# Kernel optimization log

Measured on AMD Instinct MI355X. Metric: run time of the kernel, lower is better.

The kernel has to match this reference:

```python
import jax, jax.numpy as jnp
import numpy as np

NEG_SLOPE_GAT = 0.2   # PyG GATConv default negative_slope
NEG_SLOPE_ACT = 0.01  # torch F.leaky_relu default


def gat_conv(x, src, dst, W, att_src, att_dst, b, N):
    # Single-head PyG GATConv with self-loops already appended in (src, dst).
    xl = x @ W                              # [N, d]
    a_src = xl @ att_src                    # [N]
    a_dst = xl @ att_dst                    # [N]
    e = jax.nn.leaky_relu(a_src[src] + a_dst[dst], NEG_SLOPE_GAT)  # [E]
    m = jax.ops.segment_max(e, dst, num_segments=N)                # per-dst max
    ex = jnp.exp(e - m[dst])
    s = jax.ops.segment_sum(ex, dst, num_segments=N)
    alpha = ex / (s[dst] + 1e-16)                                  # softmax over in-edges
    out = jax.ops.segment_sum(alpha[:, None] * xl[src], dst, num_segments=N)
    return out + b


def setup_inputs() -> dict:
    key = jax.random.key(0)
    ks = jax.random.split(key, 10)
    N, E, d_in, h1, h2 = 100000, 1600000, 128, 128, 64
    x = jax.random.normal(ks[0], (N, d_in), dtype=jnp.float32)
    edge_index = jax.random.randint(ks[1], (2, E), 0, N, dtype=jnp.int64)
    s1 = 1.0 / np.sqrt(d_in)
    s2 = 1.0 / np.sqrt(h1)
    W1 = jax.random.uniform(ks[2], (d_in, h1), jnp.float32, -s1, s1)
    att_src1 = jax.random.uniform(ks[3], (h1,), jnp.float32, -s2, s2)
    att_dst1 = jax.random.uniform(ks[4], (h1,), jnp.float32, -s2, s2)
    b1 = jnp.zeros((h1,), jnp.float32)
    s3 = 1.0 / np.sqrt(h2)
    W2 = jax.random.uniform(ks[5], (h1, h2), jnp.float32, -s2, s2)
    att_src2 = jax.random.uniform(ks[6], (h2,), jnp.float32, -s3, s3)
    att_dst2 = jax.random.uniform(ks[7], (h2,), jnp.float32, -s3, s3)
    b2 = jnp.zeros((h2,), jnp.float32)
    return {"x": x, "edge_index": edge_index, "W1": W1, "att_src1": att_src1,
            "att_dst1": att_dst1, "b1": b1, "W2": W2, "att_src2": att_src2,
            "att_dst2": att_dst2, "b2": b2}


def reference(x, edge_index, W1, att_src1, att_dst1, b1, W2, att_src2, att_dst2, b2):
    N = x.shape[0]
    loops = jnp.arange(N, dtype=edge_index.dtype)
    src = jnp.concatenate([edge_index[0], loops])  # add self-loops (PyG default)
    dst = jnp.concatenate([edge_index[1], loops])
    h = gat_conv(x, src, dst, W1, att_src1, att_dst1, b1, N)
    h = jax.nn.leaky_relu(h, NEG_SLOPE_ACT)
    # dropout omitted (deterministic reference / eval mode)
    h = gat_conv(h, src, dst, W2, att_src2, att_dst2, b2, N)
    return jax.nn.softmax(h, axis=0)
```

## Files before the change

kernel.cpp:

```cpp
#include <hip/hip_runtime.h>
#include <hip/hip_fp16.h>
#include <math.h>


constexpr int NPARTS = 256;
constexpr int PCAP = 8192;
constexpr int CHUNK = 4096;
constexpr int DPPMAX = 400;
constexpr int SRCB = 17;

typedef _Float16 f16x8 __attribute__((ext_vector_type(8)));
typedef float f32x4 __attribute__((ext_vector_type(4)));

__device__ __forceinline__ int bcasti(int v, int j) {
  return __builtin_amdgcn_readlane(v, j);
}
__device__ __forceinline__ float bcastf(float v, int j) {
  return __uint_as_float((unsigned)__builtin_amdgcn_readlane((int)__float_as_uint(v), j));
}
__device__ __forceinline__ __half2 xorh(__half2 v, int m) {
  int i = *(int*)&v;
  i = __shfl_xor(i, m);
  return *(__half2*)&i;
}

__global__ __launch_bounds__(256) void k_build1(
    const int* __restrict__ srcA, const int* __restrict__ dstA,
    int* __restrict__ pcur, unsigned* __restrict__ parts,
    int* __restrict__ ovf, int* __restrict__ ovf_cnt,
    const float* __restrict__ W1, const float* __restrict__ W2,
    _Float16* __restrict__ Wf1, _Float16* __restrict__ Wf2,
    int E, int N, int DPP, int nch, int ovfcap) {
  if ((int)blockIdx.x >= nch) {
    int t = ((int)blockIdx.x - nch) * 256 + (int)threadIdx.x;
    const int stride = 8 * 256;
    for (int i = t; i < 8 * 4 * 64 * 8; i += stride) {
      int j = i & 7, l = (i >> 3) & 63, kk = (i >> 9) & 3, cb = i >> 11;
      int k = kk * 32 + (l >> 4) * 8 + j, c = cb * 16 + (l & 15);
      Wf1[i] = (_Float16)W1[k * 128 + c];
    }
    for (int i = t; i < 4 * 4 * 64 * 8; i += stride) {
      int j = i & 7, l = (i >> 3) & 63, kk = (i >> 9) & 3, cb = i >> 11;
      int k = kk * 32 + (l >> 4) * 8 + j, c = cb * 16 + (l & 15);
      Wf2[i] = (_Float16)W2[k * 64 + c];
    }
    return;
  }
  __shared__ int hist[NPARTS];
  __shared__ int base[NPARTS];
  const int tot = E + N;
  const int c = blockIdx.x;
  hist[threadIdx.x] = 0;
  __syncthreads();
  const int beg = c * CHUNK;
  int pp[16], rr[16];
  unsigned pk[16];
  int dd[16], ss[16];
#pragma unroll
  for (int j = 0; j < 16; ++j) {
    int e = beg + j * 256 + (int)threadIdx.x;
    int d = -1, s = 0;
    if (e < tot) {
      if (e < E) { d = dstA[e]; s = srcA[e]; } else { d = s = e - E; }
    }
    int p = (d >= 0) ? (d / DPP) : -1;
    pp[j] = p;
    dd[j] = d; ss[j] = s;
    pk[j] = (p >= 0) ? (((unsigned)(d - p * DPP) << SRCB) | (unsigned)s) : 0u;
    rr[j] = (p >= 0) ? atomicAdd(&hist[p], 1) : 0;
  }
  __syncthreads();
  base[threadIdx.x] = atomicAdd(&pcur[threadIdx.x], hist[threadIdx.x]);
  __syncthreads();
#pragma unroll
  for (int j = 0; j < 16; ++j) {
    int p = pp[j];
    if (p < 0) continue;
    int pos = base[p] + rr[j];
    if (pos < PCAP) {
      parts[(size_t)p * PCAP + pos] = pk[j];
    } else {
      int o = atomicAdd(ovf_cnt, 1);
      if (o < ovfcap) { ovf[2 * o] = dd[j]; ovf[2 * o + 1] = ss[j]; }
    }
  }
}

template <int C, typename XT>
__device__ __forceinline__ void gemm_mfma_body(
    const XT* __restrict__ X, const _Float16* __restrict__ Wf,
    const float* __restrict__ atts, const float* __restrict__ attd,
    __half* __restrict__ XLh, float* __restrict__ a_s, float* __restrict__ a_d,
    int N, int bid) {
  constexpr int NCB = C / 16;
  const int lane = threadIdx.x & 63;
  const int wv = threadIdx.x >> 6;
  const int r0 = bid * 64 + wv * 16;
  const int arow = lane & 15;
  const int grp = lane >> 4;
  const int r = r0 + arow;
  const int rsafe = (r < N) ? r : (N - 1);

  float av[NCB], dv[NCB];
#pragma unroll
  for (int cb = 0; cb < NCB; ++cb) {
    av[cb] = atts[cb * 16 + arow];
    dv[cb] = attd[cb * 16 + arow];
  }

  f16x8 af[4];
  if constexpr (sizeof(XT) == 4) {
    const float* xr = (const float*)X + (size_t)rsafe * 128 + grp * 8;
#pragma unroll
    for (int kk = 0; kk < 4; ++kk) {
      float4 u0 = *(const float4*)(xr + kk * 32);
      float4 u1 = *(const float4*)(xr + kk * 32 + 4);
      af[kk][0] = (_Float16)u0.x; af[kk][1] = (_Float16)u0.y;
      af[kk][2] = (_Float16)u0.z; af[kk][3] = (_Float16)u0.w;
      af[kk][4] = (_Float16)u1.x; af[kk][5] = (_Float16)u1.y;
      af[kk][6] = (_Float16)u1.z; af[kk][7] = (_Float16)u1.w;
    }
  } else {
    const __half* xr = (const __half*)X + (size_t)rsafe * 128 + grp * 8;
#pragma unroll
    for (int kk = 0; kk < 4; ++kk)
      af[kk] = *(const f16x8*)(xr + kk * 32);
  }

  float ps[4] = {0.f, 0.f, 0.f, 0.f};
  float pd[4] = {0.f, 0.f, 0.f, 0.f};

#pragma unroll
  for (int cb = 0; cb < NCB; ++cb) {
    f32x4 acc = {0.f, 0.f, 0.f, 0.f};
#pragma unroll
    for (int kk = 0; kk < 4; ++kk) {
      f16x8 bf = *(const f16x8*)(Wf + ((size_t)(cb * 4 + kk) * 64 + lane) * 8);
      acc = __builtin_amdgcn_mfma_f32_16x16x32_f16(af[kk], bf, acc, 0, 0, 0);
    }
    const int ocol = cb * 16 + arow;
#pragma unroll
    for (int i = 0; i < 4; ++i) {
      const int orow = r0 + grp * 4 + i;
      if (orow < N) XLh[(size_t)orow * C + ocol] = (__half)(_Float16)acc[i];
      ps[i] = fmaf(acc[i], av[cb], ps[i]);
      pd[i] = fmaf(acc[i], dv[cb], pd[i]);
    }
  }
#pragma unroll
  for (int m = 1; m < 16; m <<= 1) {
#pragma unroll
    for (int i = 0; i < 4; ++i) {
      ps[i] += __shfl_xor(ps[i], m);
      pd[i] += __shfl_xor(pd[i], m);
    }
  }
  if (arow == 0) {
#pragma unroll
    for (int i = 0; i < 4; ++i) {
      const int orow = r0 + grp * 4 + i;
      if (orow < N) { a_s[orow] = ps[i]; a_d[orow] = pd[i]; }
    }
  }
}

struct PlaceSmem {
  int sc[NPARTS];
  int l_cnt[DPPMAX];
  int l_off[DPPMAX];
  int l_out[PCAP];
};

__global__ __launch_bounds__(256) void k_gemm1_place(
    const float* __restrict__ X, const _Float16* __restrict__ Wf,
    const float* __restrict__ atts, const float* __restrict__ attd,
    __half* __restrict__ XLh, float* __restrict__ a_s, float* __restrict__ a_d,
    int N, const unsigned* __restrict__ parts, const int* __restrict__ pcur,
    int* __restrict__ rowptr, int* __restrict__ seidx,
    int DPP, int nparts, int gb) {
  __shared__ PlaceSmem sm;
  if ((int)blockIdx.x < gb) {
    gemm_mfma_body<128, float>(X, Wf, atts, attd, XLh, a_s, a_d, N, blockIdx.x);
    return;
  }
  const int p = (int)blockIdx.x - gb;
  const int t = threadIdx.x;
  sm.sc[t] = min(pcur[t], PCAP);
  __syncthreads();
  for (int o = 1; o < NPARTS; o <<= 1) {
    int x = (t >= o) ? sm.sc[t - o] : 0;
    __syncthreads();
    sm.sc[t] += x;
    __syncthreads();
  }
  const int base = (p == 0) ? 0 : sm.sc[p - 1];
  const int n = sm.sc[p] - base;
  const int d0 = p * DPP;
  const int ndst = min(DPP, N - d0);
  const unsigned* pe = parts + (size_t)p * PCAP;

  for (int i = t; i < ndst; i += 256) sm.l_cnt[i] = 0;
  __syncthreads();
  for (int i = t; i < n; i += 256) {
    unsigned e = pe[i];
    atomicAdd(&sm.l_cnt[e >> SRCB], 1);
  }
  __syncthreads();
  if (t == 0) {
    int run = 0;
    for (int i = 0; i < ndst; ++i) { sm.l_off[i] = run; run += sm.l_cnt[i]; }
  }
  __syncthreads();
  for (int i = t; i < ndst; i += 256) {
    rowptr[d0 + i] = base + sm.l_off[i];
    sm.l_cnt[i] = sm.l_off[i];
  }
  if (p == nparts - 1 && t == 0) rowptr[N] = sm.sc[nparts - 1];
  __syncthreads();
  for (int i = t; i < n; i += 256) {
    unsigned e = pe[i];
    int pos = atomicAdd(&sm.l_cnt[e >> SRCB], 1);
    sm.l_out[pos] = (int)(e & ((1u << SRCB) - 1u));
  }
  __syncthreads();
  for (int i = t; i < n; i += 256)
    seidx[base + i] = sm.l_out[i];
}

__global__ __launch_bounds__(256) void k_gemm_l2(
    const __half* __restrict__ X, const _Float16* __restrict__ Wf,
    const float* __restrict__ atts, const float* __restrict__ attd,
    __half* __restrict__ XLh, float* __restrict__ a_s, float* __restrict__ a_d,
    int N) {
  gemm_mfma_body<64, __half>(X, Wf, atts, attd, XLh, a_s, a_d, N, blockIdx.x);
}

__global__ __launch_bounds__(256) void k_aggr_l1(
    const __half* __restrict__ XLh, const float* __restrict__ as_,
    const float* __restrict__ ad_, const int* __restrict__ rowptr,
    const int* __restrict__ seidx, const int* __restrict__ ovf,
    const int* __restrict__ ovf_cnt, const float* __restrict__ bias,
    __half* __restrict__ OUT, int N) {
  constexpr int C = 128;
  const int lane = threadIdx.x & 63;
  const int wid = threadIdx.x >> 6;
  const int grp = lane >> 5;
  const int l5 = lane & 31;
  const int novf = *ovf_cnt;
  float bb[4];
#pragma unroll
  for (int j = 0; j < 4; ++j) bb[j] = bias[4 * l5 + j];

  for (int d = blockIdx.x * 4 + wid; d < N; d += gridDim.x * 4) {
    const int beg = rowptr[d], end = rowptr[d + 1];
    const int nb = end - beg;
    const float adst = ad_[d];

    float s;
    int sv = 0; float ev = 0.f;
    if (nb <= 64) {
      if (lane < nb) {
        sv = seidx[beg + lane];
        float t = as_[sv] + adst;
        t = t > 0.f ? t : 0.2f * t;
        ev = __expf(t);
      }
      s = ev;
    } else {
      s = 0.f;
      for (int i = beg + lane; i < end; i += 64) {
        int s2 = seidx[i];
        float t = as_[s2] + adst;
        t = t > 0.f ? t : 0.2f * t;
        s += __expf(t);
      }
    }
#pragma unroll
    for (int o = 32; o; o >>= 1) s += __shfl_xor(s, o);

    if (novf > 0) {
      float so = 0.f;
      for (int i = lane; i < novf; i += 64) {
        if (ovf[2 * i] == d) {
          float t = as_[ovf[2 * i + 1]] + adst;
          t = t > 0.f ? t : 0.2f * t;
          so += __expf(t);
        }
      }
#pragma unroll
      for (int o = 32; o; o >>= 1) so += __shfl_xor(so, o);
      s += so;
    }
    const float inv = 1.f / (s + 1e-16f);

    __half2 ac01 = __floats2half2_rn(0.f, 0.f);
    __half2 ac23 = __floats2half2_rn(0.f, 0.f);
    auto pair = [&](int vsrc, float vw, int j, int cnt) {
      const int j0 = 2 * j, j1 = 2 * j + 1;
      const int s0 = bcasti(vsrc, j0);
      const float w0 = bcastf(vw, j0);
      int s1 = s0; float w1 = 0.f;
      if (j1 < cnt) { s1 = bcasti(vsrc, j1); w1 = bcastf(vw, j1); }
      const int sb = grp ? s1 : s0;
      const float wj = grp ? w1 : w0;
      const unsigned off = ((unsigned)sb << 8) + ((unsigned)l5 << 3);
      const uint2 raw = *(const uint2*)((const char*)XLh + off);
      const __half2 wh = __float2half2_rn(wj);
      ac01 = __hfma2(wh, *(const __half2*)&raw.x, ac01);
      ac23 = __hfma2(wh, *(const __half2*)&raw.y, ac23);
    };

    if (nb <= 64) {
      const float wv = ev * inv;
      const int np = (nb + 1) >> 1;
      int j = 0;
      for (; j + 4 <= np; j += 4) {
        pair(sv, wv, j, nb); pair(sv, wv, j + 1, nb);
        pair(sv, wv, j + 2, nb); pair(sv, wv, j + 3, nb);
      }
      for (; j < np; ++j) pair(sv, wv, j, nb);
    } else {
      for (int i0 = beg; i0 < end; i0 += 64) {
        const int nc = min(64, end - i0);
        int sc = 0; float wc = 0.f;
        if (lane < nc) {
          sc = seidx[i0 + lane];
          float t = as_[sc] + adst;
          t = t > 0.f ? t : 0.2f * t;
          wc = __expf(t) * inv;
        }
        const int np = (nc + 1) >> 1;
        for (int j = 0; j < np; ++j) pair(sc, wc, j, nc);
      }
    }

    ac01 = __hadd2(ac01, xorh(ac01, 32));
    ac23 = __hadd2(ac23, xorh(ac23, 32));
    float2 f01 = __half22float2(ac01);
    float2 f23 = __half22float2(ac23);
    float a0 = f01.x, a1 = f01.y, a2 = f23.x, a3 = f23.y;

    if (novf > 0) {
      for (int i = 0; i < novf; ++i) {
        if (ovf[2 * i] != d) continue;
        int os = ovf[2 * i + 1];
        float t = as_[os] + adst;
        t = t > 0.f ? t : 0.2f * t;
        float wj = __expf(t) * inv;
        const float2 raw = *(const float2*)(XLh + (size_t)os * C + l5 * 4);
        float2 x0 = __half22float2(*(const __half2*)&raw.x);
        float2 x1 = __half22float2(*(const __half2*)&raw.y);
        a0 = fmaf(wj, x0.x, a0);
        a1 = fmaf(wj, x0.y, a1);
        a2 = fmaf(wj, x1.x, a2);
        a3 = fmaf(wj, x1.y, a3);
      }
    }

    if (grp == 0) {
      float o0 = a0 + bb[0], o1 = a1 + bb[1];
      float o2 = a2 + bb[2], o3 = a3 + bb[3];
      o0 = o0 > 0.f ? o0 : 0.01f * o0;
      o1 = o1 > 0.f ? o1 : 0.01f * o1;
      o2 = o2 > 0.f ? o2 : 0.01f * o2;
      o3 = o3 > 0.f ? o3 : 0.01f * o3;
      __half2 p0 = __floats2half2_rn(o0, o1);
      __half2 p1 = __floats2half2_rn(o2, o3);
      uint2 u;
      u.x = *(unsigned*)&p0;
      u.y = *(unsigned*)&p1;
      *(uint2*)(OUT + (size_t)d * C + l5 * 4) = u;
    }
  }
}

__global__ __launch_bounds__(256) void k_aggr2(
    const __half* __restrict__ XLh, const float* __restrict__ as_,
    const float* __restrict__ ad_, const int* __restrict__ rowptr,
    const int* __restrict__ seidx, const int* __restrict__ ovf,
    const int* __restrict__ ovf_cnt, const float* __restrict__ bias,
    float* __restrict__ OUT, float* __restrict__ csum8, int N) {
  constexpr int C = 64;
  const int lane = threadIdx.x & 63;
  const int wid = threadIdx.x >> 6;
  const int q = lane >> 4;
  const int li = lane & 15;
  const int novf = *ovf_cnt;
  float bb[4];
#pragma unroll
  for (int j = 0; j < 4; ++j) bb[j] = bias[4 * li + j];
  float cs0 = 0.f, cs1 = 0.f, cs2 = 0.f, cs3 = 0.f;

  for (int d = blockIdx.x * 4 + wid; d < N; d += gridDim.x * 4) {
    const int beg = rowptr[d], end = rowptr[d + 1];
    const int nb = end - beg;
    const float adst = ad_[d];

    float s;
    int sv = 0; float ev = 0.f;
    if (nb <= 64) {
      if (lane < nb) {
        sv = seidx[beg + lane];
        float t = as_[sv] + adst;
        t = t > 0.f ? t : 0.2f * t;
        ev = __expf(t);
      }
      s = ev;
    } else {
      s = 0.f;
      for (int i = beg + lane; i < end; i += 64) {
        int s2 = seidx[i];
        float t = as_[s2] + adst;
        t = t > 0.f ? t : 0.2f * t;
        s += __expf(t);
      }
    }
#pragma unroll
    for (int o = 32; o; o >>= 1) s += __shfl_xor(s, o);

    if (novf > 0) {
      float so = 0.f;
      for (int i = lane; i < novf; i += 64) {
        if (ovf[2 * i] == d) {
          float t = as_[ovf[2 * i + 1]] + adst;
          t = t > 0.f ? t : 0.2f * t;
          so += __expf(t);
        }
      }
#pragma unroll
      for (int o = 32; o; o >>= 1) so += __shfl_xor(so, o);
      s += so;
    }
    const float inv = 1.f / (s + 1e-16f);

    __half2 ac01 = __floats2half2_rn(0.f, 0.f);
    __half2 ac23 = __floats2half2_rn(0.f, 0.f);
    auto quad = [&](int vsrc, float vw, int j, int cnt) {
      const int j0 = 4 * j;
      const int s0 = bcasti(vsrc, j0);
      const float w0 = bcastf(vw, j0);
      int s1 = s0, s2 = s0, s3 = s0;
      float w1 = 0.f, w2 = 0.f, w3 = 0.f;
      if (j0 + 1 < cnt) { s1 = bcasti(vsrc, j0 + 1); w1 = bcastf(vw, j0 + 1); }
      if (j0 + 2 < cnt) { s2 = bcasti(vsrc, j0 + 2); w2 = bcastf(vw, j0 + 2); }
      if (j0 + 3 < cnt) { s3 = bcasti(vsrc, j0 + 3); w3 = bcastf(vw, j0 + 3); }
      const int sA = (q & 1) ? s1 : s0;
      const int sB = (q & 1) ? s3 : s2;
      const int sb = (q & 2) ? sB : sA;
      const float wA = (q & 1) ? w1 : w0;
      const float wB = (q & 1) ? w3 : w2;
      const float wj = (q & 2) ? wB : wA;
      const unsigned off = ((unsigned)sb << 7) + ((unsigned)li << 3);
      const uint2 raw = *(const uint2*)((const char*)XLh + off);
      const __half2 wh = __float2half2_rn(wj);
      ac01 = __hfma2(wh, *(const __half2*)&raw.x, ac01);
      ac23 = __hfma2(wh, *(const __half2*)&raw.y, ac23);
    };

    if (nb <= 64) {
      const float wv = ev * inv;
      const int np = (nb + 3) >> 2;
      int j = 0;
      for (; j + 4 <= np; j += 4) {
        quad(sv, wv, j, nb); quad(sv, wv, j + 1, nb);
        quad(sv, wv, j + 2, nb); quad(sv, wv, j + 3, nb);
      }
      for (; j < np; ++j) quad(sv, wv, j, nb);
    } else {
      for (int i0 = beg; i0 < end; i0 += 64) {
        const int nc = min(64, end - i0);
        int sc = 0; float wc = 0.f;
        if (lane < nc) {
          sc = seidx[i0 + lane];
          float t = as_[sc] + adst;
          t = t > 0.f ? t : 0.2f * t;
          wc = __expf(t) * inv;
        }
        const int np = (nc + 3) >> 2;
        for (int j = 0; j < np; ++j) quad(sc, wc, j, nc);
      }
    }

    ac01 = __hadd2(ac01, xorh(ac01, 16));
    ac01 = __hadd2(ac01, xorh(ac01, 32));
    ac23 = __hadd2(ac23, xorh(ac23, 16));
    ac23 = __hadd2(ac23, xorh(ac23, 32));
    float2 f01 = __half22float2(ac01);
    float2 f23 = __half22float2(ac23);
    float a0 = f01.x, a1 = f01.y, a2 = f23.x, a3 = f23.y;

    if (novf > 0) {
      for (int i = 0; i < novf; ++i) {
        if (ovf[2 * i] != d) continue;
        int os = ovf[2 * i + 1];
        float t = as_[os] + adst;
        t = t > 0.f ? t : 0.2f * t;
        float wj = __expf(t) * inv;
        const float2 raw = *(const float2*)(XLh + (size_t)os * C + li * 4);
        float2 x0 = __half22float2(*(const __half2*)&raw.x);
        float2 x1 = __half22float2(*(const __half2*)&raw.y);
        a0 = fmaf(wj, x0.x, a0);
        a1 = fmaf(wj, x0.y, a1);
        a2 = fmaf(wj, x1.x, a2);
        a3 = fmaf(wj, x1.y, a3);
      }
    }

    if (q == 0) {
      float o0 = a0 + bb[0], o1 = a1 + bb[1];
      float o2 = a2 + bb[2], o3 = a3 + bb[3];
      float4 ov = make_float4(o0, o1, o2, o3);
      *(float4*)&OUT[(size_t)d * C + 4 * li] = ov;
      cs0 += __expf(o0);
      cs1 += __expf(o1);
      cs2 += __expf(o2);
      cs3 += __expf(o3);
    }
  }

  __shared__ float csA[4][64];
  if (q == 0) {
    csA[wid][4 * li + 0] = cs0;
    csA[wid][4 * li + 1] = cs1;
    csA[wid][4 * li + 2] = cs2;
    csA[wid][4 * li + 3] = cs3;
  }
  __syncthreads();
  if (threadIdx.x < 64) {
    float tot = csA[0][threadIdx.x] + csA[1][threadIdx.x] +
                csA[2][threadIdx.x] + csA[3][threadIdx.x];
    if (tot != 0.f)
      atomicAdd(&csum8[((int)blockIdx.x & 7) * 64 + (int)threadIdx.x], tot);
  }
}

__global__ void k_norm(float* __restrict__ O, const float* __restrict__ csum8,
                       size_t tot4) {
  __shared__ float cs[64];
  if (threadIdx.x < 64) {
    float s = 0.f;
#pragma unroll
    for (int r = 0; r < 8; ++r) s += csum8[r * 64 + (int)threadIdx.x];
    cs[threadIdx.x] = s;
  }
  __syncthreads();
  for (size_t i = blockIdx.x * (size_t)blockDim.x + threadIdx.x; i < tot4;
       i += (size_t)gridDim.x * blockDim.x) {
    float4 v = ((float4*)O)[i];
    int c0 = (int)((i * 4) & 63);
    v.x = __expf(v.x) / cs[c0];
    v.y = __expf(v.y) / cs[c0 + 1];
    v.z = __expf(v.z) / cs[c0 + 2];
    v.w = __expf(v.w) / cs[c0 + 3];
    ((float4*)O)[i] = v;
  }
}

extern "C" void kernel_launch(void* const* d_in, const int* in_sizes, int n_in,
                              void* d_out, int out_size, void* d_ws, size_t ws_size,
                              hipStream_t stream) {
  const float* x   = (const float*)d_in[0];
  const int*   ei  = (const int*)d_in[1];
  const float* W1  = (const float*)d_in[2];
  const float* as1 = (const float*)d_in[3];
  const float* ad1 = (const float*)d_in[4];
  const float* b1  = (const float*)d_in[5];
  const float* W2  = (const float*)d_in[6];
  const float* as2 = (const float*)d_in[7];
  const float* ad2 = (const float*)d_in[8];
  const float* b2  = (const float*)d_in[9];
  float* out = (float*)d_out;

  const int N = in_sizes[0] / 128;
  const int E = in_sizes[1] / 2;
  const int Etot = E + N;
  const int* srcA = ei;
  const int* dstA = ei + E;
  const int DPP = (N + NPARTS - 1) / NPARTS;
  const int nparts = (N + DPP - 1) / DPP;

  char* w = (char*)d_ws;
  auto take = [&](size_t bytes) -> void* {
    void* p = (void*)w;
    w += (bytes + 255) & ~(size_t)255;
    return p;
  };
  __half*    xlh   = (__half*)take((size_t)N * 128 * 2);
  __half*    xl2h  = (__half*)take((size_t)N * 64 * 2);
  __half*    h     = (__half*)take((size_t)N * 128 * 2);
  float*     a_s   = (float*)take((size_t)N * 4);
  float*     a_d   = (float*)take((size_t)N * 4);
  int*       zeroB = (int*)take((size_t)(1 + NPARTS + 512) * 4);
  int*       ovf_cnt = zeroB;
  int*       pcur    = zeroB + 1;
  float*     csum8   = (float*)(zeroB + 1 + NPARTS);
  int*       rowptr = (int*)take((size_t)(N + 1) * 4);
  int*       seidx  = (int*)take((size_t)Etot * 4);
  int*       ovf    = (int*)take((size_t)Etot * 2 * 4);
  unsigned*  parts  = (unsigned*)take((size_t)NPARTS * PCAP * 4);
  _Float16*  wf1    = (_Float16*)take((size_t)8 * 4 * 64 * 8 * 2);
  _Float16*  wf2    = (_Float16*)take((size_t)4 * 4 * 64 * 8 * 2);

  hipMemsetAsync(zeroB, 0, (size_t)(1 + NPARTS + 512) * 4, stream);

  const int nch = (Etot + CHUNK - 1) / CHUNK;
  const int gb = (N + 63) / 64;

  k_build1<<<nch + 8, 256, 0, stream>>>(srcA, dstA, pcur, parts, ovf, ovf_cnt,
                                        W1, W2, wf1, wf2, E, N, DPP, nch, Etot);
  k_gemm1_place<<<gb + NPARTS, 256, 0, stream>>>(
      x, wf1, as1, ad1, xlh, a_s, a_d, N, parts, pcur, rowptr, seidx,
      DPP, nparts, gb);
  k_aggr_l1<<<8192, 256, 0, stream>>>(xlh, a_s, a_d, rowptr, seidx, ovf, ovf_cnt,
                                      b1, h, N);
  k_gemm_l2<<<gb, 256, 0, stream>>>(h, wf2, as2, ad2, xl2h, a_s, a_d, N);
  k_aggr2<<<8192, 256, 0, stream>>>(xl2h, a_s, a_d, rowptr, seidx, ovf, ovf_cnt,
                                    b2, out, csum8, N);
  const size_t tot4 = (size_t)N * 64 / 4;
  k_norm<<<2048, 256, 0, stream>>>(out, csum8, tot4);
}
```

Measured before the change: 218.4 us.

## Process four edges per wave step with 16-byte gathers in layer-1 aggregation

The layer-1 aggregation kernel now splits each wave into four 16-lane groups that each gather 8 half values (16 bytes) per edge, so one step handles four edges instead of two. This halves the number of broadcast-and-gather iterations and widens the loads, at the cost of an extra cross-lane reduction stage and more registers. Separately, layer 2 now stores exp(out) directly, and the normalization kernel multiplies by a precomputed reciprocal column sum instead of recomputing exp and dividing.

```diff
diff --git a/kernel.cpp b/kernel.cpp
--- a/kernel.cpp
+++ b/kernel.cpp
@@ -244,12 +244,12 @@
   constexpr int C = 128;
   const int lane = threadIdx.x & 63;
   const int wid = threadIdx.x >> 6;
-  const int grp = lane >> 5;
-  const int l5 = lane & 31;
+  const int q = lane >> 4;
+  const int li = lane & 15;
   const int novf = *ovf_cnt;
-  float bb[4];
-#pragma unroll
-  for (int j = 0; j < 4; ++j) bb[j] = bias[4 * l5 + j];
+  float bb[8];
+#pragma unroll
+  for (int j = 0; j < 8; ++j) bb[j] = bias[8 * li + j];
 
   for (int d = blockIdx.x * 4 + wid; d < N; d += gridDim.x * 4) {
     const int beg = rowptr[d], end = rowptr[d + 1];
@@ -295,30 +295,41 @@
 
     __half2 ac01 = __floats2half2_rn(0.f, 0.f);
     __half2 ac23 = __floats2half2_rn(0.f, 0.f);
-    auto pair = [&](int vsrc, float vw, int j, int cnt) {
-      const int j0 = 2 * j, j1 = 2 * j + 1;
+    __half2 ac45 = __floats2half2_rn(0.f, 0.f);
+    __half2 ac67 = __floats2half2_rn(0.f, 0.f);
+    auto quad = [&](int vsrc, float vw, int j, int cnt) {
+      const int j0 = 4 * j;
       const int s0 = bcasti(vsrc, j0);
       const float w0 = bcastf(vw, j0);
-      int s1 = s0; float w1 = 0.f;
-      if (j1 < cnt) { s1 = bcasti(vsrc, j1); w1 = bcastf(vw, j1); }
-      const int sb = grp ? s1 : s0;
-      const float wj = grp ? w1 : w0;
-      const unsigned off = ((unsigned)sb << 8) + ((unsigned)l5 << 3);
-      const uint2 raw = *(const uint2*)((const char*)XLh + off);
+      int s1 = s0, s2 = s0, s3 = s0;
+      float w1 = 0.f, w2 = 0.f, w3 = 0.f;
+      if (j0 + 1 < cnt) { s1 = bcasti(vsrc, j0 + 1); w1 = bcastf(vw, j0 + 1); }
+      if (j0 + 2 < cnt) { s2 = bcasti(vsrc, j0 + 2); w2 = bcastf(vw, j0 + 2); }
+      if (j0 + 3 < cnt) { s3 = bcasti(vsrc, j0 + 3); w3 = bcastf(vw, j0 + 3); }
+      const int sA = (q & 1) ? s1 : s0;
+      const int sB = (q & 1) ? s3 : s2;
+      const int sb = (q & 2) ? sB : sA;
+      const float wA = (q & 1) ? w1 : w0;
+      const float wB = (q & 1) ? w3 : w2;
+      const float wj = (q & 2) ? wB : wA;
+      const unsigned off = ((unsigned)sb << 8) + ((unsigned)li << 4);
+      const uint4 raw = *(const uint4*)((const char*)XLh + off);
       const __half2 wh = __float2half2_rn(wj);
       ac01 = __hfma2(wh, *(const __half2*)&raw.x, ac01);
       ac23 = __hfma2(wh, *(const __half2*)&raw.y, ac23);
+      ac45 = __hfma2(wh, *(const __half2*)&raw.z, ac45);
+      ac67 = __hfma2(wh, *(const __half2*)&raw.w, ac67);
     };
 
     if (nb <= 64) {
       const float wv = ev * inv;
-      const int np = (nb + 1) >> 1;
+      const int np = (nb + 3) >> 2;
       int j = 0;
       for (; j + 4 <= np; j += 4) {
-        pair(sv, wv, j, nb); pair(sv, wv, j + 1, nb);
-        pair(sv, wv, j + 2, nb); pair(sv, wv, j + 3, nb);
-      }
-      for (; j < np; ++j) pair(sv, wv, j, nb);
+        quad(sv, wv, j, nb); quad(sv, wv, j + 1, nb);
+        quad(sv, wv, j + 2, nb); quad(sv, wv, j + 3, nb);
+      }
+      for (; j < np; ++j) quad(sv, wv, j, nb);
     } else {
       for (int i0 = beg; i0 < end; i0 += 64) {
         const int nc = min(64, end - i0);
@@ -329,16 +340,24 @@
           t = t > 0.f ? t : 0.2f * t;
           wc = __expf(t) * inv;
         }
-        const int np = (nc + 1) >> 1;
-        for (int j = 0; j < np; ++j) pair(sc, wc, j, nc);
-      }
-    }
-
+        const int np = (nc + 3) >> 2;
+        for (int j = 0; j < np; ++j) quad(sc, wc, j, nc);
+      }
+    }
+
+    ac01 = __hadd2(ac01, xorh(ac01, 16));
     ac01 = __hadd2(ac01, xorh(ac01, 32));
+    ac23 = __hadd2(ac23, xorh(ac23, 16));
     ac23 = __hadd2(ac23, xorh(ac23, 32));
+    ac45 = __hadd2(ac45, xorh(ac45, 16));
+    ac45 = __hadd2(ac45, xorh(ac45, 32));
+    ac67 = __hadd2(ac67, xorh(ac67, 16));
+    ac67 = __hadd2(ac67, xorh(ac67, 32));
     float2 f01 = __half22float2(ac01);
     float2 f23 = __half22float2(ac23);
-    float a0 = f01.x, a1 = f01.y, a2 = f23.x, a3 = f23.y;
+    float2 f45 = __half22float2(ac45);
+    float2 f67 = __half22float2(ac67);
+    float a[8] = {f01.x, f01.y, f23.x, f23.y, f45.x, f45.y, f67.x, f67.y};
 
     if (novf > 0) {
       for (int i = 0; i < novf; ++i) {
@@ -347,29 +366,28 @@
         float t = as_[os] + adst;
         t = t > 0.f ? t : 0.2f * t;
         float wj = __expf(t) * inv;
-        const float2 raw = *(const float2*)(XLh + (size_t)os * C + l5 * 4);
-        float2 x0 = __half22float2(*(const __half2*)&raw.x);
-        float2 x1 = __half22float2(*(const __half2*)&raw.y);
-        a0 = fmaf(wj, x0.x, a0);
-        a1 = fmaf(wj, x0.y, a1);
-        a2 = fmaf(wj, x1.x, a2);
-        a3 = fmaf(wj, x1.y, a3);
-      }
-    }
-
-    if (grp == 0) {
-      float o0 = a0 + bb[0], o1 = a1 + bb[1];
-      float o2 = a2 + bb[2], o3 = a3 + bb[3];
-      o0 = o0 > 0.f ? o0 : 0.01f * o0;
-      o1 = o1 > 0.f ? o1 : 0.01f * o1;
-      o2 = o2 > 0.f ? o2 : 0.01f * o2;
-      o3 = o3 > 0.f ? o3 : 0.01f * o3;
-      __half2 p0 = __floats2half2_rn(o0, o1);
-      __half2 p1 = __floats2half2_rn(o2, o3);
-      uint2 u;
-      u.x = *(unsigned*)&p0;
-      u.y = *(unsigned*)&p1;
-      *(uint2*)(OUT + (size_t)d * C + l5 * 4) = u;
+        const float4 raw = *(const float4*)(XLh + (size_t)os * C + li * 8);
+        const __half2* hp = (const __half2*)&raw;
+#pragma unroll
+        for (int k = 0; k < 4; ++k) {
+          float2 xv = __half22float2(hp[k]);
+          a[2 * k] = fmaf(wj, xv.x, a[2 * k]);
+          a[2 * k + 1] = fmaf(wj, xv.y, a[2 * k + 1]);
+        }
+      }
+    }
+
+    if (q == 0) {
+      __half2 pk[4];
+#pragma unroll
+      for (int k = 0; k < 4; ++k) {
+        float o0 = a[2 * k] + bb[2 * k];
+        float o1 = a[2 * k + 1] + bb[2 * k + 1];
+        o0 = o0 > 0.f ? o0 : 0.01f * o0;
+        o1 = o1 > 0.f ? o1 : 0.01f * o1;
+        pk[k] = __floats2half2_rn(o0, o1);
+      }
+      *(uint4*)(OUT + (size_t)d * C + li * 8) = *(uint4*)pk;
     }
   }
 }
@@ -507,14 +525,15 @@
     }
 
     if (q == 0) {
-      float o0 = a0 + bb[0], o1 = a1 + bb[1];
-      float o2 = a2 + bb[2], o3 = a3 + bb[3];
-      float4 ov = make_float4(o0, o1, o2, o3);
-      *(float4*)&OUT[(size_t)d * C + 4 * li] = ov;
-      cs0 += __expf(o0);
-      cs1 += __expf(o1);
-      cs2 += __expf(o2);
-      cs3 += __expf(o3);
+      float e0 = __expf(a0 + bb[0]);
+      float e1 = __expf(a1 + bb[1]);
+      float e2 = __expf(a2 + bb[2]);
+      float e3 = __expf(a3 + bb[3]);
+      *(float4*)&OUT[(size_t)d * C + 4 * li] = make_float4(e0, e1, e2, e3);
+      cs0 += e0;
+      cs1 += e1;
+      cs2 += e2;
+      cs3 += e3;
     }
   }
 
@@ -541,17 +560,17 @@
     float s = 0.f;
 #pragma unroll
     for (int r = 0; r < 8; ++r) s += csum8[r * 64 + (int)threadIdx.x];
-    cs[threadIdx.x] = s;
+    cs[threadIdx.x] = 1.f / s;
   }
   __syncthreads();
   for (size_t i = blockIdx.x * (size_t)blockDim.x + threadIdx.x; i < tot4;
        i += (size_t)gridDim.x * blockDim.x) {
     float4 v = ((float4*)O)[i];
     int c0 = (int)((i * 4) & 63);
-    v.x = __expf(v.x) / cs[c0];
-    v.y = __expf(v.y) / cs[c0 + 1];
-    v.z = __expf(v.z) / cs[c0 + 2];
-    v.w = __expf(v.w) / cs[c0 + 3];
+    v.x *= cs[c0];
+    v.y *= cs[c0 + 1];
+    v.z *= cs[c0 + 2];
+    v.w *= cs[c0 + 3];
     ((float4*)O)[i] = v;
   }
 }
```

Result: no change. 219.4 us (+0.4%).
